# Kernel tuning notes

Hardware: AMD Instinct MI355X
Metric: run time of the kernel (lower is better)

Reference implementation:

```python
import jax, jax.numpy as jnp
import numpy as np

BSZ, SEQ, DIM = 4, 4096, 1024
MEASURE_DIM = 64
TOPK = 16
NUM_TARGETS = 1


def fwht(x):
    """Fast Walsh-Hadamard transform over last dim (power of two), orthonormal scaling."""
    n = x.shape[-1]
    y = x
    h = 1
    while h < n:
        y = y.reshape(*y.shape[:-1], -1, 2, h)
        a, b = y[..., 0, :], y[..., 1, :]
        y = jnp.concatenate((a + b, a - b), axis=-1)
        y = y.reshape(*x.shape[:-1], n)
        h *= 2
    return y * (n ** -0.5)


def setup_inputs() -> dict:
    key = jax.random.key(0)
    kx, kg, ka, kt, ks, kp = jax.random.split(key, 6)
    x = jax.random.normal(kx, (BSZ, SEQ, DIM), dtype=jnp.float32)
    gates = jax.random.uniform(kg, (BSZ, NUM_TARGETS, MEASURE_DIM), dtype=jnp.float32) + 0.5
    alpha = jax.random.uniform(ka, (BSZ, NUM_TARGETS, 1), dtype=jnp.float32) * 0.1
    tau = jax.random.uniform(kt, (BSZ, NUM_TARGETS, 1), dtype=jnp.float32) * 0.02
    signs = jnp.where(jax.random.uniform(ks, (DIM,)) > 0.5, 1.0, -1.0).astype(jnp.float32)
    perm = jax.random.permutation(kp, DIM).astype(jnp.int32)
    inv_perm = jnp.argsort(perm).astype(jnp.int32)
    return {"x": x, "gates": gates, "alpha": alpha, "tau": tau,
            "signs": signs, "perm": perm, "inv_perm": inv_perm, "target_idx": 0}


def reference(x, gates, alpha, tau, signs, perm, inv_perm, target_idx):
    signs_ = signs.astype(x.dtype)
    # ---- sense: sign flip -> permute -> FWHT -> truncate ----
    y = jnp.take((x * signs_[None, None, :]), perm, axis=-1)
    z = fwht(y)[..., :MEASURE_DIM]  # [B, S, m]
    # ---- shrink (topk mode) ----
    gate = gates[:, target_idx][:, None, :]            # [B, 1, m]
    alpha_t = alpha[:, target_idx][:, None, :]         # [B, 1, 1]
    tau_t = jnp.abs(tau[:, target_idx])[:, None, :]    # [B, 1, 1]
    gated = gate * z
    agated = jnp.abs(gated)
    _, idx = jax.lax.top_k(agated, TOPK)               # [B, S, k]
    mask = jax.nn.one_hot(idx, MEASURE_DIM, dtype=gated.dtype).sum(-2)  # [B, S, m]
    sparse = jnp.where((mask > 0) & (agated >= tau_t), gated, jnp.zeros_like(gated))
    zs = alpha_t * sparse
    # ---- reconstruct: pad -> FWHT -> inverse permute -> sign flip ----
    full = jnp.zeros((*zs.shape[:-1], DIM), dtype=zs.dtype).at[..., :MEASURE_DIM].set(zs)
    r = jnp.take(fwht(full), inv_perm, axis=-1) * signs_[None, None, :]
    return x + r
```

## Files before the change

kernel.cpp:

```cpp
#include <hip/hip_runtime.h>

#define SEQ 4096
#define DIM 1024
#define MD 64
#define TOPK 16
#define RPB 4

__global__ __launch_bounds__(256) void csa_kernel(
    const float* __restrict__ x,
    const float* __restrict__ gates,
    const float* __restrict__ alpha,
    const float* __restrict__ tau,
    const float* __restrict__ signs,
    const int*   __restrict__ perm,
    const int*   __restrict__ inv_perm,
    const int*   __restrict__ target_idx,
    float*       __restrict__ out)
{
    __shared__ float y[RPB][DIM];

    const int t    = threadIdx.x;
    const int lane = t & 63;
    const int wv   = t >> 6;
    const int row  = (blockIdx.x << 2) | wv;
    const int b    = row >> 12;

    const float* xr = x + (size_t)row * DIM;

    #pragma unroll
    for (int c = 0; c < 4; ++c) {
        const float4 xv = ((const float4*)xr)[c * 64 + lane];
        const float4 sg = ((const float4*)signs)[c * 64 + lane];
        float4 yv;
        yv.x = xv.x * sg.x; yv.y = xv.y * sg.y;
        yv.z = xv.z * sg.z; yv.w = xv.w * sg.w;
        ((float4*)y[wv])[c * 64 + lane] = yv;
    }

    int pidx[16];
    #pragma unroll
    for (int k = 0; k < 16; ++k) pidx[k] = perm[lane + 64 * k];
    float s = 0.f;
    #pragma unroll
    for (int k = 0; k < 16; ++k) s += y[wv][pidx[k]];

    float v = s;
    #pragma unroll
    for (int bit = 1; bit < MD; bit <<= 1) {
        const float o = __shfl_xor(v, bit, MD);
        v = (lane & bit) ? (o - v) : (v + o);
    }

    const int   ti   = target_idx[0];
    const float gate = gates[(b + ti) * MD + lane];
    const float g    = gate * v * 0.03125f;
    const float ag   = fabsf(g);

    const unsigned ka = __float_as_uint(ag);
    unsigned T = 0u;
    #pragma unroll
    for (int bit = 30; bit >= 0; --bit) {
        const unsigned cand = T | (1u << bit);
        if (__popcll(__ballot(ka >= cand)) >= TOPK) T = cand;
    }
    const int ngt = __popcll(__ballot(ka > T));
    const unsigned long long eq = __ballot(ka == T);
    const int eqrank = __popcll(eq & ((1ull << lane) - 1ull));
    const bool keep = (ka > T) || ((ka == T) && (eqrank < TOPK - ngt));

    const float tauv = fabsf(tau[b + ti]);
    const float al   = alpha[b + ti];
    float zs = (keep && ag >= tauv) ? al * g : 0.f;

    #pragma unroll
    for (int bit = 1; bit < MD; bit <<= 1) {
        const float o = __shfl_xor(zs, bit, MD);
        zs = (lane & bit) ? (o - zs) : (zs + o);
    }
    const float w = zs * 0.03125f;
    const int   wbits = __float_as_int(w);

    float* outr = out + (size_t)row * DIM;
    #pragma unroll
    for (int c = 0; c < 4; ++c) {
        const float4 yv = ((const float4*)y[wv])[c * 64 + lane];
        const float4 sg = ((const float4*)signs)[c * 64 + lane];
        const int4   ip = ((const int4*)inv_perm)[c * 64 + lane];
        float4 ov;
        ov.x = sg.x * (yv.x + __int_as_float(__builtin_amdgcn_ds_bpermute((ip.x & 63) << 2, wbits)));
        ov.y = sg.y * (yv.y + __int_as_float(__builtin_amdgcn_ds_bpermute((ip.y & 63) << 2, wbits)));
        ov.z = sg.z * (yv.z + __int_as_float(__builtin_amdgcn_ds_bpermute((ip.z & 63) << 2, wbits)));
        ov.w = sg.w * (yv.w + __int_as_float(__builtin_amdgcn_ds_bpermute((ip.w & 63) << 2, wbits)));
        ((float4*)outr)[c * 64 + lane] = ov;
    }
}

extern "C" void kernel_launch(void* const* d_in, const int* in_sizes, int n_in,
                              void* d_out, int out_size, void* d_ws, size_t ws_size,
                              hipStream_t stream) {
    const float* x        = (const float*)d_in[0];
    const float* gates    = (const float*)d_in[1];
    const float* alpha    = (const float*)d_in[2];
    const float* tau      = (const float*)d_in[3];
    const float* signs    = (const float*)d_in[4];
    const int*   perm     = (const int*)d_in[5];
    const int*   inv_perm = (const int*)d_in[6];
    const int*   tgt      = (const int*)d_in[7];
    float*       out      = (float*)d_out;

    const int rows = (4 * SEQ);
    csa_kernel<<<rows / RPB, 256, 0, stream>>>(x, gates, alpha, tau, signs,
                                               perm, inv_perm, tgt, out);
}
```

Before: 127.5 us.

## Process four rows per wave with software-prefetched next row

```diff
diff --git a/kernel.cpp b/kernel.cpp
--- a/kernel.cpp
+++ b/kernel.cpp
@@ -4,9 +4,10 @@
 #define DIM 1024
 #define MD 64
 #define TOPK 16
-#define RPB 4
+#define WPB 4
+#define RPW 4
 
-__global__ __launch_bounds__(256) void csa_kernel(
+__global__ __launch_bounds__(WPB * 64) void csa_kernel(
     const float* __restrict__ x,
     const float* __restrict__ gates,
     const float* __restrict__ alpha,
@@ -17,81 +18,98 @@
     const int*   __restrict__ target_idx,
     float*       __restrict__ out)
 {
-    __shared__ float y[RPB][DIM];
+    __shared__ float y[WPB][DIM];
 
-    const int t    = threadIdx.x;
-    const int lane = t & 63;
-    const int wv   = t >> 6;
-    const int row  = (blockIdx.x << 2) | wv;
-    const int b    = row >> 12;
+    const int lane = threadIdx.x & 63;
+    const int wv   = threadIdx.x >> 6;
+    const int base = (blockIdx.x * WPB + wv) * RPW;
+    const int b    = base >> 12;
 
-    const float* xr = x + (size_t)row * DIM;
+    const float4* x4  = (const float4*)x;
+    const float4* sg4 = (const float4*)signs;
+    const int4*   ip4 = (const int4*)inv_perm;
 
-    #pragma unroll
-    for (int c = 0; c < 4; ++c) {
-        const float4 xv = ((const float4*)xr)[c * 64 + lane];
-        const float4 sg = ((const float4*)signs)[c * 64 + lane];
-        float4 yv;
-        yv.x = xv.x * sg.x; yv.y = xv.y * sg.y;
-        yv.z = xv.z * sg.z; yv.w = xv.w * sg.w;
-        ((float4*)y[wv])[c * 64 + lane] = yv;
-    }
-
+    const int   ti   = target_idx[0];
+    const float gate = gates[(b + ti) * MD + lane];
+    const float tauv = fabsf(tau[b + ti]);
+    const float al   = alpha[b + ti];
     int pidx[16];
     #pragma unroll
     for (int k = 0; k < 16; ++k) pidx[k] = perm[lane + 64 * k];
-    float s = 0.f;
+
+    float4 xv[4];
     #pragma unroll
-    for (int k = 0; k < 16; ++k) s += y[wv][pidx[k]];
-
-    float v = s;
-    #pragma unroll
-    for (int bit = 1; bit < MD; bit <<= 1) {
-        const float o = __shfl_xor(v, bit, MD);
-        v = (lane & bit) ? (o - v) : (v + o);
-    }
-
-    const int   ti   = target_idx[0];
-    const float gate = gates[(b + ti) * MD + lane];
-    const float g    = gate * v * 0.03125f;
-    const float ag   = fabsf(g);
-
-    const unsigned ka = __float_as_uint(ag);
-    unsigned T = 0u;
-    #pragma unroll
-    for (int bit = 30; bit >= 0; --bit) {
-        const unsigned cand = T | (1u << bit);
-        if (__popcll(__ballot(ka >= cand)) >= TOPK) T = cand;
-    }
-    const int ngt = __popcll(__ballot(ka > T));
-    const unsigned long long eq = __ballot(ka == T);
-    const int eqrank = __popcll(eq & ((1ull << lane) - 1ull));
-    const bool keep = (ka > T) || ((ka == T) && (eqrank < TOPK - ngt));
-
-    const float tauv = fabsf(tau[b + ti]);
-    const float al   = alpha[b + ti];
-    float zs = (keep && ag >= tauv) ? al * g : 0.f;
+    for (int c = 0; c < 4; ++c)
+        xv[c] = x4[(size_t)base * (DIM / 4) + c * 64 + lane];
 
     #pragma unroll
-    for (int bit = 1; bit < MD; bit <<= 1) {
-        const float o = __shfl_xor(zs, bit, MD);
-        zs = (lane & bit) ? (o - zs) : (zs + o);
-    }
-    const float w = zs * 0.03125f;
-    const int   wbits = __float_as_int(w);
+    for (int r = 0; r < RPW; ++r) {
+        #pragma unroll
+        for (int c = 0; c < 4; ++c) {
+            const float4 sg = sg4[c * 64 + lane];
+            float4 yv;
+            yv.x = xv[c].x * sg.x; yv.y = xv[c].y * sg.y;
+            yv.z = xv[c].z * sg.z; yv.w = xv[c].w * sg.w;
+            ((float4*)y[wv])[c * 64 + lane] = yv;
+        }
 
-    float* outr = out + (size_t)row * DIM;
-    #pragma unroll
-    for (int c = 0; c < 4; ++c) {
-        const float4 yv = ((const float4*)y[wv])[c * 64 + lane];
-        const float4 sg = ((const float4*)signs)[c * 64 + lane];
-        const int4   ip = ((const int4*)inv_perm)[c * 64 + lane];
-        float4 ov;
-        ov.x = sg.x * (yv.x + __int_as_float(__builtin_amdgcn_ds_bpermute((ip.x & 63) << 2, wbits)));
-        ov.y = sg.y * (yv.y + __int_as_float(__builtin_amdgcn_ds_bpermute((ip.y & 63) << 2, wbits)));
-        ov.z = sg.z * (yv.z + __int_as_float(__builtin_amdgcn_ds_bpermute((ip.z & 63) << 2, wbits)));
-        ov.w = sg.w * (yv.w + __int_as_float(__builtin_amdgcn_ds_bpermute((ip.w & 63) << 2, wbits)));
-        ((float4*)outr)[c * 64 + lane] = ov;
+        float4 xn[4];
+        if (r + 1 < RPW) {
+            #pragma unroll
+            for (int c = 0; c < 4; ++c)
+                xn[c] = x4[(size_t)(base + r + 1) * (DIM / 4) + c * 64 + lane];
+        }
+
+        float s = 0.f;
+        #pragma unroll
+        for (int k = 0; k < 16; ++k) s += y[wv][pidx[k]];
+
+        float v = s;
+        #pragma unroll
+        for (int bit = 1; bit < MD; bit <<= 1) {
+            const float o = __shfl_xor(v, bit, 64);
+            v = (lane & bit) ? (o - v) : (v + o);
+        }
+        const float g  = gate * v * 0.03125f;
+        const float ag = fabsf(g);
+
+        const unsigned ka = __float_as_uint(ag);
+        unsigned T = 0u;
+        #pragma unroll
+        for (int bit = 30; bit >= 0; --bit) {
+            const unsigned cand = T | (1u << bit);
+            if (__popcll(__ballot(ka >= cand)) >= TOPK) T = cand;
+        }
+        const int ngt = __popcll(__ballot(ka > T));
+        const int erk = __popcll(__ballot(ka == T) & ((1ull << lane) - 1ull));
+        const bool keep = (ka > T) || ((ka == T) && (erk < TOPK - ngt));
+
+        float zs = (keep && ag >= tauv) ? al * g : 0.f;
+
+        #pragma unroll
+        for (int bit = 1; bit < MD; bit <<= 1) {
+            const float o = __shfl_xor(zs, bit, 64);
+            zs = (lane & bit) ? (o - zs) : (zs + o);
+        }
+        const int wb = __float_as_int(zs * 0.03125f);
+
+        float* outr = out + (size_t)(base + r) * DIM;
+        #pragma unroll
+        for (int c = 0; c < 4; ++c) {
+            const float4 sg = sg4[c * 64 + lane];
+            const int4   ip = ip4[c * 64 + lane];
+            float4 o;
+            o.x = xv[c].x + sg.x * __int_as_float(__builtin_amdgcn_ds_bpermute((ip.x & 63) << 2, wb));
+            o.y = xv[c].y + sg.y * __int_as_float(__builtin_amdgcn_ds_bpermute((ip.y & 63) << 2, wb));
+            o.z = xv[c].z + sg.z * __int_as_float(__builtin_amdgcn_ds_bpermute((ip.z & 63) << 2, wb));
+            o.w = xv[c].w + sg.w * __int_as_float(__builtin_amdgcn_ds_bpermute((ip.w & 63) << 2, wb));
+            ((float4*)outr)[c * 64 + lane] = o;
+        }
+
+        if (r + 1 < RPW) {
+            #pragma unroll
+            for (int c = 0; c < 4; ++c) xv[c] = xn[c];
+        }
     }
 }
 
@@ -108,7 +126,7 @@
     const int*   tgt      = (const int*)d_in[7];
     float*       out      = (float*)d_out;
 
-    const int rows = (4 * SEQ);
-    csa_kernel<<<rows / RPB, 256, 0, stream>>>(x, gates, alpha, tau, signs,
-                                               perm, inv_perm, tgt, out);
+    const int rows = 4 * SEQ;
+    csa_kernel<<<rows / (WPB * RPW), WPB * 64, 0, stream>>>(
+        x, gates, alpha, tau, signs, perm, inv_perm, tgt, out);
 }
```

Result: slower. 130.8 us (+2.6%).
